# Kernel tuning notes

Measured on AMD Instinct MI355X. Metric: run time of the kernel, lower is better.

Reference implementation:

```python
import jax, jax.numpy as jnp
import numpy as np

IN_FEATURES = 4096
B, S = 4, 4096


def setup_inputs() -> dict:
    key = jax.random.key(0)
    k1, k2, k3 = jax.random.split(key, 3)
    input_1 = jax.random.normal(k1, (B, S, IN_FEATURES), dtype=jnp.float32)
    input_2 = jax.random.normal(k2, (B, S, IN_FEATURES), dtype=jnp.float32)
    weight = jax.random.uniform(k3, (IN_FEATURES,), dtype=jnp.float32)
    return {"input_1": input_1, "input_2": input_2, "weight": weight}


def reference(input_1, input_2, weight):
    # Original: linear(input_1, diag(w)) + linear(input_2, diag(1-w)).
    # diag(w) is symmetric, so x @ diag(w).T == x * w (elementwise broadcast
    # over the last feature axis) -- identical math without the O(n^2) matmul.
    return input_1 * weight + input_2 * (1.0 - weight)
```

## Files before the change

kernel.cpp:

```cpp
#include <hip/hip_runtime.h>


typedef float fvec4 __attribute__((ext_vector_type(4)));

__global__ __launch_bounds__(256) void merger_kernel(
    const fvec4* __restrict__ a,
    const fvec4* __restrict__ b,
    const fvec4* __restrict__ w,
    fvec4* __restrict__ out) {
    const int t = threadIdx.x;
    const int base = blockIdx.x * 1024 + t;

    const fvec4 wv0 = w[t];
    const fvec4 wv1 = w[t + 256];
    const fvec4 wv2 = w[t + 512];
    const fvec4 wv3 = w[t + 768];

    const fvec4 av0 = a[base];
    const fvec4 av1 = a[base + 256];
    const fvec4 av2 = a[base + 512];
    const fvec4 av3 = a[base + 768];
    const fvec4 bv0 = b[base];
    const fvec4 bv1 = b[base + 256];
    const fvec4 bv2 = b[base + 512];
    const fvec4 bv3 = b[base + 768];

    const fvec4 o0 = av0 * wv0 + bv0 * (1.0f - wv0);
    const fvec4 o1 = av1 * wv1 + bv1 * (1.0f - wv1);
    const fvec4 o2 = av2 * wv2 + bv2 * (1.0f - wv2);
    const fvec4 o3 = av3 * wv3 + bv3 * (1.0f - wv3);

    __builtin_nontemporal_store(o0, &out[base]);
    __builtin_nontemporal_store(o1, &out[base + 256]);
    __builtin_nontemporal_store(o2, &out[base + 512]);
    __builtin_nontemporal_store(o3, &out[base + 768]);
}

extern "C" void kernel_launch(void* const* d_in, const int* in_sizes, int n_in,
                              void* d_out, int out_size, void* d_ws, size_t ws_size,
                              hipStream_t stream) {
    const fvec4* a = (const fvec4*)d_in[0];
    const fvec4* b = (const fvec4*)d_in[1];
    const fvec4* w = (const fvec4*)d_in[2];
    fvec4* out = (fvec4*)d_out;
    const int grid = out_size / (4 * 1024);
    merger_kernel<<<grid, 256, 0, stream>>>(a, b, w, out);
}
```

Baseline: 139.6 us.

## Process eight rows per block with software-pipelined double-buffered loads

```diff
diff --git a/kernel.cpp b/kernel.cpp
--- a/kernel.cpp
+++ b/kernel.cpp
@@ -9,31 +9,66 @@
     const fvec4* __restrict__ w,
     fvec4* __restrict__ out) {
     const int t = threadIdx.x;
-    const int base = blockIdx.x * 1024 + t;
+    const int base = blockIdx.x * 8192 + t;
 
-    const fvec4 wv0 = w[t];
-    const fvec4 wv1 = w[t + 256];
-    const fvec4 wv2 = w[t + 512];
-    const fvec4 wv3 = w[t + 768];
+    const fvec4 w0 = w[t];
+    const fvec4 w1 = w[t + 256];
+    const fvec4 w2 = w[t + 512];
+    const fvec4 w3 = w[t + 768];
 
-    const fvec4 av0 = a[base];
-    const fvec4 av1 = a[base + 256];
-    const fvec4 av2 = a[base + 512];
-    const fvec4 av3 = a[base + 768];
-    const fvec4 bv0 = b[base];
-    const fvec4 bv1 = b[base + 256];
-    const fvec4 bv2 = b[base + 512];
-    const fvec4 bv3 = b[base + 768];
+    fvec4 A0, A1, A2, A3;
+    fvec4 B0, B1, B2, B3;
 
-    const fvec4 o0 = av0 * wv0 + bv0 * (1.0f - wv0);
-    const fvec4 o1 = av1 * wv1 + bv1 * (1.0f - wv1);
-    const fvec4 o2 = av2 * wv2 + bv2 * (1.0f - wv2);
-    const fvec4 o3 = av3 * wv3 + bv3 * (1.0f - wv3);
+    A0 = a[base];
+    A1 = a[base + 256];
+    A2 = b[base];
+    A3 = b[base + 256];
 
-    __builtin_nontemporal_store(o0, &out[base]);
-    __builtin_nontemporal_store(o1, &out[base + 256]);
-    __builtin_nontemporal_store(o2, &out[base + 512]);
-    __builtin_nontemporal_store(o3, &out[base + 768]);
+#pragma unroll 1
+    for (int k = 0; k < 7; ++k) {
+        const int e = base + k * 1024;
+        const int o = e + 512;
+
+        B0 = a[o];
+        B1 = a[o + 256];
+        B2 = b[o];
+        B3 = b[o + 256];
+
+        fvec4 r0 = A0 * w0 + A2 * (1.0f - w0);
+        fvec4 r1 = A1 * w1 + A3 * (1.0f - w1);
+        __builtin_nontemporal_store(r0, &out[e]);
+        __builtin_nontemporal_store(r1, &out[e + 256]);
+
+        const int e2 = e + 1024;
+        A0 = a[e2];
+        A1 = a[e2 + 256];
+        A2 = b[e2];
+        A3 = b[e2 + 256];
+
+        fvec4 r2 = B0 * w2 + B2 * (1.0f - w2);
+        fvec4 r3 = B1 * w3 + B3 * (1.0f - w3);
+        __builtin_nontemporal_store(r2, &out[o]);
+        __builtin_nontemporal_store(r3, &out[o + 256]);
+    }
+
+    {
+        const int e = base + 7 * 1024;
+        const int o = e + 512;
+        B0 = a[o];
+        B1 = a[o + 256];
+        B2 = b[o];
+        B3 = b[o + 256];
+
+        fvec4 r0 = A0 * w0 + A2 * (1.0f - w0);
+        fvec4 r1 = A1 * w1 + A3 * (1.0f - w1);
+        __builtin_nontemporal_store(r0, &out[e]);
+        __builtin_nontemporal_store(r1, &out[e + 256]);
+
+        fvec4 r2 = B0 * w2 + B2 * (1.0f - w2);
+        fvec4 r3 = B1 * w3 + B3 * (1.0f - w3);
+        __builtin_nontemporal_store(r2, &out[o]);
+        __builtin_nontemporal_store(r3, &out[o + 256]);
+    }
 }
 
 extern "C" void kernel_launch(void* const* d_in, const int* in_sizes, int n_in,
@@ -43,6 +78,6 @@
     const fvec4* b = (const fvec4*)d_in[1];
     const fvec4* w = (const fvec4*)d_in[2];
     fvec4* out = (fvec4*)d_out;
-    const int grid = out_size / (4 * 1024);
+    const int grid = out_size / (4 * 8192);
     merger_kernel<<<grid, 256, 0, stream>>>(a, b, w, out);
 }
```

After: 161.7 us. +15.9%, slower.
